# Optimization experiments

Measured on AMD Instinct MI355X. Metric: run time of the kernel, lower is better.

The kernel has to match this reference:

```python
import jax, jax.numpy as jnp
import numpy as np

B, S, H, NH = 4, 1024, 2048, 32
HD = H // NH
EPS = 1e-5

def layer_norm(x, w, b):
    mu = jnp.mean(x, axis=-1, keepdims=True)
    var = jnp.mean(jnp.square(x - mu), axis=-1, keepdims=True)
    return (x - mu) * jax.lax.rsqrt(var + EPS) * w + b

def setup_inputs() -> dict:
    key = jax.random.key(0)
    ks = jax.random.split(key, 8)
    s = 0.02
    inp = {
        'hidden_states': jax.random.normal(ks[0], (B, S, H), jnp.float32),
        'mask': jnp.tril(jnp.ones((S, S), jnp.float32))[None, None],  # causal 0/1
        'ln1_w': jnp.ones((H,), jnp.float32), 'ln1_b': jnp.zeros((H,), jnp.float32),
        'w_qkv': s * jax.random.normal(ks[1], (H, 3 * H), jnp.float32),
        'b_qkv': jnp.zeros((3 * H,), jnp.float32),
        'w_dense': s * jax.random.normal(ks[2], (H, H), jnp.float32),
        'b_dense': jnp.zeros((H,), jnp.float32),
        'ln3_w': jnp.ones((H,), jnp.float32), 'ln3_b': jnp.zeros((H,), jnp.float32),
        'ln2_w': jnp.ones((H,), jnp.float32), 'ln2_b': jnp.zeros((H,), jnp.float32),
        'w_h4h': s * jax.random.normal(ks[3], (H, 4 * H), jnp.float32),
        'b_h4h': jnp.zeros((4 * H,), jnp.float32),
        'w_4hh': s * jax.random.normal(ks[4], (4 * H, H), jnp.float32),
        'b_4hh': jnp.zeros((H,), jnp.float32),
        'ln4_w': jnp.ones((H,), jnp.float32), 'ln4_b': jnp.zeros((H,), jnp.float32),
    }
    return inp

def _layer(hidden_states, mask, ln1_w, ln1_b, w_qkv, b_qkv, w_dense, b_dense,
           ln3_w, ln3_b, ln2_w, ln2_b, w_h4h, b_h4h, w_4hh, b_4hh, ln4_w, ln4_b):
    # --- input LN ---
    x1 = layer_norm(hidden_states, ln1_w, ln1_b)
    # --- self attention ---
    qkv = x1 @ w_qkv + b_qkv                              # [B,S,3H]
    q, k, v = jnp.split(qkv, 3, axis=-1)
    def heads(t):  # [B,S,H] -> [B,NH,S,HD]
        return t.reshape(B, S, NH, HD).transpose(0, 2, 1, 3)
    q, k, v = heads(q), heads(k), heads(v)
    scores = jnp.einsum('bnqd,bnkd->bnqk', q / jnp.sqrt(jnp.float32(HD)), k)
    scores = scores * mask - 10000.0 * (1.0 - mask)
    probs = jax.nn.softmax(scores, axis=-1)
    ctx = jnp.einsum('bnqk,bnkd->bnqd', probs, v)
    ctx = ctx.transpose(0, 2, 1, 3).reshape(B, S, H)
    attn_out = ctx @ w_dense + b_dense
    # sandwich LN on attention output
    attn_out = layer_norm(attn_out, ln3_w, ln3_b)
    ln_input = hidden_states + attn_out
    # --- MLP ---
    x2 = layer_norm(ln_input, ln2_w, ln2_b)
    inter = jax.nn.gelu(x2 @ w_h4h + b_h4h, approximate=True)
    mlp_out = inter @ w_4hh + b_4hh
    mlp_out = layer_norm(mlp_out, ln4_w, ln4_b)
    return ln_input + mlp_out

def reference(hidden_states, mask, ln1_w, ln1_b, w_qkv, b_qkv, w_dense, b_dense,
              ln3_w, ln3_b, ln2_w, ln2_b, w_h4h, b_h4h, w_4hh, b_4hh, ln4_w, ln4_b):
    return _layer(hidden_states, mask, ln1_w, ln1_b, w_qkv, b_qkv, w_dense, b_dense,
                  ln3_w, ln3_b, ln2_w, ln2_b, w_h4h, b_h4h, w_4hh, b_4hh, ln4_w, ln4_b)
```

## Files before the change

### kernel.cpp

```cpp
#include <hip/hip_runtime.h>
#include <cstdint>
#include <cstddef>

typedef __bf16 bf16_t;
typedef __bf16 bf16x8 __attribute__((ext_vector_type(8)));
typedef float f32x4 __attribute__((ext_vector_type(4)));

#define BB 4
#define SS 1024
#define HH 2048
#define NHH 32
#define HDD 64
#define MTOK 4096

static constexpr size_t OFF_WQKV   = 0;
static constexpr size_t OFF_WDENSE = 25165824;
static constexpr size_t OFF_WH4H   = 33554432;
static constexpr size_t OFF_W4HH   = 67108864;
static constexpr size_t OFF_X1     = 100663296;
static constexpr size_t OFF_QKV    = 117440512;
static constexpr size_t OFF_ATTND2 = 150994944;
static constexpr size_t OFF_VT     = 167772160;
static constexpr size_t OFF_LNIN   = 184549376;
static constexpr size_t OFF_MLP    = 218103808;
static constexpr size_t OFF_MLP2   = 0;

__device__ __forceinline__ uint16_t f2bfu(float f) {
  union { float f; uint32_t u; } v; v.f = f;
  return (uint16_t)((v.u + 0x7FFFu + ((v.u >> 16) & 1u)) >> 16);
}
__device__ __forceinline__ bf16_t f2bf(float f) {
  union { uint16_t u; bf16_t b; } o; o.u = f2bfu(f);
  return o.b;
}

__device__ __forceinline__ void g2l16(const void* g, void* l) {
  __builtin_amdgcn_global_load_lds(
      (const __attribute__((address_space(1))) void*)g,
      (__attribute__((address_space(3))) void*)l, 16, 0, 0);
}

__global__ void convert_transpose_kernel(const float* __restrict__ W, bf16_t* __restrict__ WT,
                                         int K, int N) {
  __shared__ float t[32][33];
  const int n0 = blockIdx.x * 32;
  const int k0 = blockIdx.y * 32;
  const int tx = threadIdx.x, ty = threadIdx.y;
#pragma unroll
  for (int j = 0; j < 4; ++j)
    t[ty + j * 8][tx] = W[(size_t)(k0 + ty + j * 8) * N + n0 + tx];
  __syncthreads();
#pragma unroll
  for (int j = 0; j < 4; ++j)
    WT[(size_t)(n0 + ty + j * 8) * K + k0 + tx] = f2bf(t[tx][ty + j * 8]);
}

__global__ void transpose_v_kernel(const bf16_t* __restrict__ v, bf16_t* __restrict__ vT) {
  __shared__ bf16_t t[32][33];
  const int s0 = blockIdx.x * 32;
  const int d0 = blockIdx.y * 32;
  const size_t bh = blockIdx.z;
  const int tx = threadIdx.x, ty = threadIdx.y;
  const bf16_t* src = v + bh * (size_t)SS * HDD;
#pragma unroll
  for (int j = 0; j < 4; ++j)
    t[ty + j * 8][tx] = src[(size_t)(s0 + ty + j * 8) * HDD + d0 + tx];
  __syncthreads();
  bf16_t* dst = vT + bh * (size_t)HDD * SS;
#pragma unroll
  for (int j = 0; j < 4; ++j)
    dst[(size_t)(d0 + ty + j * 8) * SS + s0 + tx] = t[tx][ty + j * 8];
}

__device__ __forceinline__ void block_reduce2(float& s, float& ss) {
#pragma unroll
  for (int o = 32; o > 0; o >>= 1) {
    s += __shfl_down(s, o, 64);
    ss += __shfl_down(ss, o, 64);
  }
  __shared__ float red[8];
  const int wave = threadIdx.x >> 6;
  const int lane = threadIdx.x & 63;
  if (lane == 0) { red[wave] = s; red[4 + wave] = ss; }
  __syncthreads();
  s = red[0] + red[1] + red[2] + red[3];
  ss = red[4] + red[5] + red[6] + red[7];
  __syncthreads();
}

__device__ __forceinline__ void load8(const float* base, int tid, float* v) {
  float4 a = ((const float4*)base)[tid];
  float4 b = ((const float4*)base)[tid + 256];
  v[0] = a.x; v[1] = a.y; v[2] = a.z; v[3] = a.w;
  v[4] = b.x; v[5] = b.y; v[6] = b.z; v[7] = b.w;
}
__device__ __forceinline__ void store8f(float* base, int tid, const float* v) {
  ((float4*)base)[tid] = make_float4(v[0], v[1], v[2], v[3]);
  ((float4*)base)[tid + 256] = make_float4(v[4], v[5], v[6], v[7]);
}
__device__ __forceinline__ void store8bf(bf16_t* base, int tid, const float* v) {
  ushort4 o0 = {f2bfu(v[0]), f2bfu(v[1]), f2bfu(v[2]), f2bfu(v[3])};
  ushort4 o1 = {f2bfu(v[4]), f2bfu(v[5]), f2bfu(v[6]), f2bfu(v[7])};
  ((ushort4*)base)[tid] = o0;
  ((ushort4*)base)[tid + 256] = o1;
}
__device__ __forceinline__ void row_stats(const float* v, float& mean, float& inv) {
  float s = 0.f, ss = 0.f;
#pragma unroll
  for (int i = 0; i < 8; ++i) { s += v[i]; ss += v[i] * v[i]; }
  block_reduce2(s, ss);
  mean = s * (1.0f / 2048.0f);
  float var = ss * (1.0f / 2048.0f) - mean * mean;
  inv = rsqrtf(var + 1e-5f);
}

__global__ __launch_bounds__(256) void ln1_kernel(const float* __restrict__ x,
                                                  const float* __restrict__ w,
                                                  const float* __restrict__ b,
                                                  bf16_t* __restrict__ out) {
  const int row = blockIdx.x, tid = threadIdx.x;
  float v[8], wv[8], bv[8], o[8];
  load8(x + (size_t)row * HH, tid, v);
  float mean, inv;
  row_stats(v, mean, inv);
  load8(w, tid, wv);
  load8(b, tid, bv);
#pragma unroll
  for (int i = 0; i < 8; ++i) o[i] = (v[i] - mean) * inv * wv[i] + bv[i];
  store8bf(out + (size_t)row * HH, tid, o);
}

__global__ __launch_bounds__(256) void fuse_mid_kernel(
    const float* __restrict__ ad, const float* __restrict__ ad2,
    const float* __restrict__ hid,
    const float* __restrict__ w3, const float* __restrict__ b3,
    const float* __restrict__ w2, const float* __restrict__ b2,
    float* __restrict__ lnin, bf16_t* __restrict__ x2) {
  const int row = blockIdx.x, tid = threadIdx.x;
  float a[8], a2[8], h[8], wv[8], bv[8], l[8], o[8];
  load8(ad + (size_t)row * HH, tid, a);
  load8(ad2 + (size_t)row * HH, tid, a2);
#pragma unroll
  for (int i = 0; i < 8; ++i) a[i] += a2[i];
  float mean3, inv3;
  row_stats(a, mean3, inv3);
  load8(hid + (size_t)row * HH, tid, h);
  load8(w3, tid, wv);
  load8(b3, tid, bv);
#pragma unroll
  for (int i = 0; i < 8; ++i) l[i] = h[i] + (a[i] - mean3) * inv3 * wv[i] + bv[i];
  store8f(lnin + (size_t)row * HH, tid, l);
  float mean2, inv2;
  row_stats(l, mean2, inv2);
  load8(w2, tid, wv);
  load8(b2, tid, bv);
#pragma unroll
  for (int i = 0; i < 8; ++i) o[i] = (l[i] - mean2) * inv2 * wv[i] + bv[i];
  store8bf(x2 + (size_t)row * HH, tid, o);
}

__global__ __launch_bounds__(256) void fuse_out_kernel(
    const float* __restrict__ mlp, const float* __restrict__ mlp2,
    const float* __restrict__ lnin,
    const float* __restrict__ w4, const float* __restrict__ b4,
    float* __restrict__ out) {
  const int row = blockIdx.x, tid = threadIdx.x;
  float m[8], m2[8], l[8], wv[8], bv[8], o[8];
  load8(mlp + (size_t)row * HH, tid, m);
  load8(mlp2 + (size_t)row * HH, tid, m2);
#pragma unroll
  for (int i = 0; i < 8; ++i) m[i] += m2[i];
  float mean4, inv4;
  row_stats(m, mean4, inv4);
  load8(lnin + (size_t)row * HH, tid, l);
  load8(w4, tid, wv);
  load8(b4, tid, bv);
#pragma unroll
  for (int i = 0; i < 8; ++i) o[i] = l[i] + (m[i] - mean4) * inv4 * wv[i] + bv[i];
  store8f(out + (size_t)row * HH, tid, o);
}

#define MFMA16(a, b, cc) __builtin_amdgcn_mfma_f32_16x16x32_bf16(a, b, cc, 0, 0, 0)

#define STAGE(ISB, BUF, HALF, KT) do {                                              \
    const char* _s = ((ISB) ? bPan : aPan) + (size_t)((HALF) * 128) * ldb +         \
                     (size_t)(KT) * 128 + scb;                                      \
    char* _d = lds + ((ISB) ? 65536 : 0) + (BUF) * 32768 + (HALF) * 16384 +         \
               wave * 1024;                                                         \
    g2l16(_s + (size_t)srow * ldb, _d);                                             \
    g2l16(_s + (size_t)(srow + 64) * ldb, _d + 8192);                               \
  } while (0)

#define LDA(BUF, MQ)                                                                \
  _Pragma("unroll") for (int mf = 0; mf < 4; ++mf) {                                \
    const char* _p = aRd + (BUF) * 32768 + (MQ) * 8192 + mf * 2048;                 \
    aR[mf * 2]     = *(const bf16x8*)(_p + colK0);                                  \
    aR[mf * 2 + 1] = *(const bf16x8*)(_p + colK1);                                  \
  }

#define LDB(BR, BUF, NQ)                                                            \
  _Pragma("unroll") for (int nf = 0; nf < 2; ++nf) {                                \
    const char* _p = bRd + (BUF) * 32768 + (NQ) * 4096 + nf * 2048;                 \
    BR[nf * 2]     = *(const bf16x8*)(_p + colK0);                                  \
    BR[nf * 2 + 1] = *(const bf16x8*)(_p + colK1);                                  \
  }

#define MMA(MQ, NQ, BR)                                                             \
  _Pragma("unroll") for (int mf = 0; mf < 4; ++mf)                                  \
  _Pragma("unroll") for (int nf = 0; nf < 2; ++nf)                                  \
  _Pragma("unroll") for (int ks = 0; ks < 2; ++ks)                                  \
    acc[(MQ) * 4 + mf][(NQ) * 2 + nf] =                                             \
        MFMA16(aR[mf * 2 + ks], BR[nf * 2 + ks], acc[(MQ) * 4 + mf][(NQ) * 2 + nf]);

#define BARS()                                                                      \
  __builtin_amdgcn_sched_barrier(0);                                                \
  __builtin_amdgcn_s_barrier();                                                     \
  __builtin_amdgcn_s_setprio(1);

#define ENDP()                                                                      \
  __builtin_amdgcn_s_setprio(0);                                                    \
  __builtin_amdgcn_sched_barrier(0);                                                \
  __builtin_amdgcn_s_barrier();

template <int EPI, int SPLITK>
__global__ __launch_bounds__(512, 2) void gemm256(
    const bf16_t* __restrict__ A, const bf16_t* __restrict__ BT,
    const float* __restrict__ bias, void* __restrict__ out0, void* __restrict__ out1,
    const int M, const int N, const int Keff, const int ldK) {
  __shared__ alignas(16) char lds[131072];
  const int tid = threadIdx.x;
  const int wave = tid >> 6, lane = tid & 63;
  const int wm = wave >> 2, wn = wave & 3;
  const int c = lane & 15, g = lane >> 4;

  const int nwg = gridDim.x;
  int bid = (blockIdx.x & 7) * (nwg >> 3) + (blockIdx.x >> 3);
  const int nm = M >> 8;
  int slice = 0;
  if (SPLITK == 2) {
    const int per = nm * (N >> 8);
    slice = bid >= per;
    bid -= slice * per;
  }
  const int mt = bid % nm, nt = bid / nm;

  const size_t ldb = (size_t)ldK * 2;
  const char* aPan = (const char*)A + (size_t)(mt * 256) * ldb + (size_t)(slice * Keff) * 2;
  const char* bPan = (const char*)BT + (size_t)(nt * 256) * ldb + (size_t)(slice * Keff) * 2;

  const int srow = tid >> 3;
  const int scb = ((tid & 7) << 4) ^ ((srow & 7) << 4);

  const int x4 = (c & 7) << 4;
  const int colK0 = (g * 16) ^ x4;
  const int colK1 = (64 + g * 16) ^ x4;
  const char* aRd = lds + wm * 16384 + c * 128;
  const char* bRd = lds + 65536 + (wn >> 1) * 16384 + ((wn & 1) * 64 + c) * 128;

  f32x4 acc[8][4] = {};
  bf16x8 aR[8], b0R[4], b1R[4];

  const int NITER = Keff >> 7;
  const int NT2 = NITER * 2;

  STAGE(1, 0, 0, 0); STAGE(1, 0, 1, 0); STAGE(0, 0, 0, 0); STAGE(0, 0, 1, 0);
  STAGE(1, 1, 0, 1); STAGE(1, 1, 1, 1);
  asm volatile("s_waitcnt vmcnt(4)" ::: "memory");
  __builtin_amdgcn_sched_barrier(0);
  __builtin_amdgcn_s_barrier();

  for (int it = 0; it < NITER; ++it) {
    const int ktb = 2 * it + 1;
    int kt2 = 2 * it + 2; if (kt2 >= NT2) kt2 = 0;
    int kt3 = 2 * it + 3; if (kt3 >= NT2) kt3 = 0;
    LDA(0, 0); LDB(b0R, 0, 0); STAGE(0, 1, 0, ktb);
    BARS(); MMA(0, 0, b0R); ENDP();
    LDB(b1R, 0, 1); STAGE(0, 1, 1, ktb);
    BARS(); MMA(0, 1, b1R); ENDP();
    LDA(0, 1); STAGE(1, 0, 0, kt2);
    BARS(); MMA(1, 1, b1R); ENDP();
    STAGE(1, 0, 1, kt2);
    asm volatile("s_waitcnt vmcnt(4)" ::: "memory");
    BARS(); MMA(1, 0, b0R); ENDP();
    LDA(1, 0); LDB(b0R, 1, 0); STAGE(0, 0, 0, kt2);
    BARS(); MMA(0, 0, b0R); ENDP();
    LDB(b1R, 1, 1); STAGE(0, 0, 1, kt2);
    BARS(); MMA(0, 1, b1R); ENDP();
    LDA(1, 1); STAGE(1, 1, 0, kt3);
    BARS(); MMA(1, 1, b1R); ENDP();
    STAGE(1, 1, 1, kt3);
    asm volatile("s_waitcnt vmcnt(4)" ::: "memory");
    BARS(); MMA(1, 0, b0R); ENDP();
  }

  const int rowb = mt * 256 + wm * 128 + g * 4;
  const int colb = nt * 256 + wn * 64 + c;
  if constexpr (EPI == 0) {
    float* o = (float*)(slice ? out1 : out0);
#pragma unroll
    for (int nf = 0; nf < 4; ++nf) {
      const int col = colb + nf * 16;
      const float bv = (slice == 0) ? bias[col] : 0.0f;
#pragma unroll
      for (int mf = 0; mf < 8; ++mf) {
        const int r = rowb + mf * 16;
#pragma unroll
        for (int e = 0; e < 4; ++e)
          o[(size_t)(r + e) * N + col] = acc[mf][nf][e] + bv;
      }
    }
  } else if constexpr (EPI == 1) {
    bf16_t* o = (bf16_t*)out0;
#pragma unroll
    for (int nf = 0; nf < 4; ++nf) {
      const int col = colb + nf * 16;
      const float bv = bias[col];
      const int which = col >> 11;
      const int hh = (col & 2047) >> 6;
      const int dd = col & 63;
#pragma unroll
      for (int mf = 0; mf < 8; ++mf) {
        const int r = rowb + mf * 16;
#pragma unroll
        for (int e = 0; e < 4; ++e) {
          const int rr2 = r + e;
          const int bb = rr2 >> 10;
          const int sq = rr2 & 1023;
          o[(size_t)which * 8388608 +
            ((((size_t)bb * NHH + hh) * SS + sq) * HDD + dd)] = f2bf(acc[mf][nf][e] + bv);
        }
      }
    }
  } else {
    bf16_t* o = (bf16_t*)out0;
#pragma unroll
    for (int nf = 0; nf < 4; ++nf) {
      const int col = colb + nf * 16;
      const float bv = bias[col];
#pragma unroll
      for (int mf = 0; mf < 8; ++mf) {
        const int r = rowb + mf * 16;
#pragma unroll
        for (int e = 0; e < 4; ++e) {
          float u = acc[mf][nf][e] + bv;
          float cc2 = 0.7978845608f * (u + 0.044715f * u * u * u);
          float ex = __expf(2.0f * cc2);
          float th = 1.0f - 2.0f / (ex + 1.0f);
          o[(size_t)(r + e) * N + col] = f2bf(0.5f * u * (1.0f + th));
        }
      }
    }
  }
}

__global__ __launch_bounds__(512) void attn_kernel(
    const bf16_t* __restrict__ q, const bf16_t* __restrict__ k,
    const bf16_t* __restrict__ vT, bf16_t* __restrict__ ctx) {
  __shared__ alignas(16) char Ksm[8192];
  __shared__ alignas(16) char Vsm[8192];
  __shared__ alignas(16) char Psm[16384];

  const int id = blockIdx.x;
  const int qt = 7 - (id >> 7);
  const int bh = id & 127;
  const int tid = threadIdx.x;
  const int wave = tid >> 6;
  const int lane = tid & 63;
  const int q0 = qt * 128;
  const int q0w = q0 + wave * 16;
  const int c = lane & 15;
  const int g = lane >> 4;

  const bf16_t* qb = q + ((size_t)bh * SS + q0w) * HDD;
  const bf16x8 qa0 = *(const bf16x8*)(qb + c * HDD + g * 8);
  const bf16x8 qa1 = *(const bf16x8*)(qb + c * HDD + 32 + g * 8);

  f32x4 o[4] = {};
  float mrow[4], lrow[4];
#pragma unroll
  for (int e = 0; e < 4; ++e) { mrow[e] = -1e30f; lrow[e] = 0.0f; }

  const int sr = tid >> 3;
  const int sgb = ((tid & 7) * 16) ^ ((sr & 7) << 4);
  const char* kgb = (const char*)(k + (size_t)bh * SS * HDD);
  const char* vgb = (const char*)(vT + (size_t)bh * HDD * SS);
  char* kdst = Ksm + wave * 1024;
  char* vdst = Vsm + wave * 1024;
  char* Pw = Psm + wave * 2048;

  const int ntiles = (q0 + 128) >> 6;

  for (int t = 0; t < ntiles; ++t) {
    const int kb = t * 64;
    g2l16(kgb + (size_t)(kb + sr) * 128 + sgb, kdst);
    g2l16(vgb + (size_t)sr * 2048 + (size_t)kb * 2 + sgb, vdst);
    __syncthreads();

    if (kb < q0w + 16) {
      f32x4 s[4] = {};
#pragma unroll
      for (int sub = 0; sub < 4; ++sub) {
        const int n = sub * 16 + c;
        const int x = (n & 7) << 4;
        bf16x8 kf0 = *(const bf16x8*)(Ksm + n * 128 + ((g * 16) ^ x));
        bf16x8 kf1 = *(const bf16x8*)(Ksm + n * 128 + ((64 + g * 16) ^ x));
        s[sub] = MFMA16(qa0, kf0, s[sub]);
        s[sub] = MFMA16(qa1, kf1, s[sub]);
      }
      const bool diag = (kb + 63 > q0w);
      float pv[4][4];
#pragma unroll
      for (int sub = 0; sub < 4; ++sub)
#pragma unroll
        for (int e = 0; e < 4; ++e) {
          float sv = s[sub][e] * 0.125f;
          if (diag && (kb + sub * 16 + c > q0w + g * 4 + e)) sv = -10000.0f;
          pv[sub][e] = sv;
        }
      float scale[4];
#pragma unroll
      for (int e = 0; e < 4; ++e) {
        float mx = fmaxf(fmaxf(pv[0][e], pv[1][e]), fmaxf(pv[2][e], pv[3][e]));
        mx = fmaxf(mx, __shfl_xor(mx, 1, 64));
        mx = fmaxf(mx, __shfl_xor(mx, 2, 64));
        mx = fmaxf(mx, __shfl_xor(mx, 4, 64));
        mx = fmaxf(mx, __shfl_xor(mx, 8, 64));
        const float mnew = fmaxf(mrow[e], mx);
        scale[e] = __expf(mrow[e] - mnew);
        mrow[e] = mnew;
      }
#pragma unroll
      for (int e = 0; e < 4; ++e) {
        const int row = g * 4 + e;
        const int xr = (row & 7) << 4;
        float sum = 0.0f;
#pragma unroll
        for (int sub = 0; sub < 4; ++sub) {
          float p = __expf(pv[sub][e] - mrow[e]);
          sum += p;
          const int cb = (sub * 16 + c) * 2;
          *(bf16_t*)(Pw + row * 128 + (cb ^ xr)) = f2bf(p);
        }
        sum += __shfl_xor(sum, 1, 64);
        sum += __shfl_xor(sum, 2, 64);
        sum += __shfl_xor(sum, 4, 64);
        sum += __shfl_xor(sum, 8, 64);
        lrow[e] = lrow[e] * scale[e] + sum;
      }
#pragma unroll
      for (int d = 0; d < 4; ++d)
#pragma unroll
        for (int e = 0; e < 4; ++e) o[d][e] *= scale[e];
      const int xa = (c & 7) << 4;
      bf16x8 pa0 = *(const bf16x8*)(Pw + c * 128 + ((g * 16) ^ xa));
      bf16x8 pa1 = *(const bf16x8*)(Pw + c * 128 + ((64 + g * 16) ^ xa));
#pragma unroll
      for (int d = 0; d < 4; ++d) {
        const int n = d * 16 + c;
        const int xv = (n & 7) << 4;
        bf16x8 vf0 = *(const bf16x8*)(Vsm + n * 128 + ((g * 16) ^ xv));
        bf16x8 vf1 = *(const bf16x8*)(Vsm + n * 128 + ((64 + g * 16) ^ xv));
        o[d] = MFMA16(pa0, vf0, o[d]);
        o[d] = MFMA16(pa1, vf1, o[d]);
      }
    }
    __syncthreads();
  }

  const int b = bh >> 5, h = bh & 31;
#pragma unroll
  for (int e = 0; e < 4; ++e) {
    const int qrow = q0w + g * 4 + e;
    const float inv = 1.0f / lrow[e];
#pragma unroll
    for (int d = 0; d < 4; ++d)
      ctx[((size_t)b * SS + qrow) * HH + h * 64 + d * 16 + c] = f2bf(o[d][e] * inv);
  }
}

extern "C" void kernel_launch(void* const* d_in, const int* in_sizes, int n_in,
                              void* d_out, int out_size, void* d_ws, size_t ws_size,
                              hipStream_t stream) {
  const float* hidden = (const float*)d_in[0];
  const float* ln1w = (const float*)d_in[2];
  const float* ln1b = (const float*)d_in[3];
  const float* wqkv = (const float*)d_in[4];
  const float* bqkv = (const float*)d_in[5];
  const float* wdense = (const float*)d_in[6];
  const float* bdense = (const float*)d_in[7];
  const float* ln3w = (const float*)d_in[8];
  const float* ln3b = (const float*)d_in[9];
  const float* ln2w = (const float*)d_in[10];
  const float* ln2b = (const float*)d_in[11];
  const float* wh4h = (const float*)d_in[12];
  const float* bh4h = (const float*)d_in[13];
  const float* w4hh = (const float*)d_in[14];
  const float* b4hh = (const float*)d_in[15];
  const float* ln4w = (const float*)d_in[16];
  const float* ln4b = (const float*)d_in[17];

  char* ws = (char*)d_ws;
  bf16_t* wqkvT = (bf16_t*)(ws + OFF_WQKV);
  bf16_t* wdenseT = (bf16_t*)(ws + OFF_WDENSE);
  bf16_t* wh4hT = (bf16_t*)(ws + OFF_WH4H);
  bf16_t* w4hhT = (bf16_t*)(ws + OFF_W4HH);
  bf16_t* x1 = (bf16_t*)(ws + OFF_X1);
  bf16_t* qkv = (bf16_t*)(ws + OFF_QKV);
  bf16_t* qp = qkv;
  bf16_t* kp = qkv + 8388608;
  bf16_t* vp = qkv + 2 * 8388608;
  bf16_t* vT = (bf16_t*)(ws + OFF_VT);
  bf16_t* ctx = (bf16_t*)(ws + OFF_X1);
  float* attnd = (float*)(ws + OFF_QKV);
  float* attnd2 = (float*)(ws + OFF_ATTND2);
  float* lnin = (float*)(ws + OFF_LNIN);
  bf16_t* x2 = (bf16_t*)(ws + OFF_X1);
  bf16_t* inter = (bf16_t*)(ws + OFF_QKV);
  float* mlp = (float*)(ws + OFF_MLP);
  float* mlp2 = (float*)(ws + OFF_MLP2);

  dim3 tb(32, 8);
  convert_transpose_kernel<<<dim3(6144 / 32, 2048 / 32), tb, 0, stream>>>(wqkv, wqkvT, 2048, 6144);
  convert_transpose_kernel<<<dim3(2048 / 32, 2048 / 32), tb, 0, stream>>>(wdense, wdenseT, 2048, 2048);
  convert_transpose_kernel<<<dim3(8192 / 32, 2048 / 32), tb, 0, stream>>>(wh4h, wh4hT, 2048, 8192);
  convert_transpose_kernel<<<dim3(2048 / 32, 8192 / 32), tb, 0, stream>>>(w4hh, w4hhT, 8192, 2048);

  ln1_kernel<<<MTOK, 256, 0, stream>>>(hidden, ln1w, ln1b, x1);

  gemm256<1, 1><<<dim3((6144 / 256) * (4096 / 256)), 512, 0, stream>>>(
      x1, wqkvT, bqkv, (void*)qp, nullptr, MTOK, 6144, 2048, 2048);

  transpose_v_kernel<<<dim3(SS / 32, HDD / 32, BB * NHH), tb, 0, stream>>>(vp, vT);

  attn_kernel<<<dim3(1024), 512, 0, stream>>>(qp, kp, vT, ctx);

  gemm256<0, 2><<<dim3((2048 / 256) * (4096 / 256) * 2), 512, 0, stream>>>(
      ctx, wdenseT, bdense, (void*)attnd, (void*)attnd2, MTOK, 2048, 1024, 2048);

  fuse_mid_kernel<<<MTOK, 256, 0, stream>>>(attnd, attnd2, hidden, ln3w, ln3b, ln2w, ln2b, lnin, x2);

  gemm256<2, 1><<<dim3((8192 / 256) * (4096 / 256)), 512, 0, stream>>>(
      x2, wh4hT, bh4h, (void*)inter, nullptr, MTOK, 8192, 2048, 2048);

  gemm256<0, 2><<<dim3((2048 / 256) * (4096 / 256) * 2), 512, 0, stream>>>(
      inter, w4hhT, b4hh, (void*)mlp, (void*)mlp2, MTOK, 2048, 4096, 8192);

  fuse_out_kernel<<<MTOK, 256, 0, stream>>>(mlp, mlp2, lnin, ln4w, ln4b, (float*)d_out);
}
```

Baseline: 639.8 us.

## Restructure GEMM LDS prefetch schedule to deeper full-tile lookahead

Reorders the global-to-LDS staging so that both A and B halves of a whole k-tile are prefetched one full tile ahead, with all eight stages issued in the prologue and a vmcnt(8) wait in place of vmcnt(4). The loads are grouped so they are issued in clusters after the phases that finish reading each buffer. The sched_barrier calls around the MFMA phases are removed, which gives the compiler more freedom to interleave instructions. The aim is to hide global memory latency better. The cost is more loads in flight and a higher risk of LDS hazards if the buffer reuse order is wrong.

```diff
diff --git a/kernel.cpp b/kernel.cpp
--- a/kernel.cpp
+++ b/kernel.cpp
@@ -212,15 +212,15 @@
     acc[(MQ) * 4 + mf][(NQ) * 2 + nf] =                                             \
         MFMA16(aR[mf * 2 + ks], BR[nf * 2 + ks], acc[(MQ) * 4 + mf][(NQ) * 2 + nf]);
 
-#define BARS()                                                                      \
-  __builtin_amdgcn_sched_barrier(0);                                                \
+#define PH()                                                                        \
   __builtin_amdgcn_s_barrier();                                                     \
-  __builtin_amdgcn_s_setprio(1);
-
-#define ENDP()                                                                      \
+  __builtin_amdgcn_s_setprio(1)
+
+#define PE()                                                                        \
   __builtin_amdgcn_s_setprio(0);                                                    \
-  __builtin_amdgcn_sched_barrier(0);                                                \
-  __builtin_amdgcn_s_barrier();
+  __builtin_amdgcn_s_barrier()
+
+#define VM8() asm volatile("s_waitcnt vmcnt(8)" ::: "memory")
 
 template <int EPI, int SPLITK>
 __global__ __launch_bounds__(512, 2) void gemm256(
@@ -263,34 +263,34 @@
   const int NITER = Keff >> 7;
   const int NT2 = NITER * 2;
 
-  STAGE(1, 0, 0, 0); STAGE(1, 0, 1, 0); STAGE(0, 0, 0, 0); STAGE(0, 0, 1, 0);
+  STAGE(0, 0, 0, 0); STAGE(0, 0, 1, 0);
+  STAGE(1, 0, 0, 0); STAGE(1, 0, 1, 0);
+  STAGE(0, 1, 0, 1); STAGE(0, 1, 1, 1);
   STAGE(1, 1, 0, 1); STAGE(1, 1, 1, 1);
-  asm volatile("s_waitcnt vmcnt(4)" ::: "memory");
-  __builtin_amdgcn_sched_barrier(0);
+  VM8();
   __builtin_amdgcn_s_barrier();
 
   for (int it = 0; it < NITER; ++it) {
-    const int ktb = 2 * it + 1;
-    int kt2 = 2 * it + 2; if (kt2 >= NT2) kt2 = 0;
-    int kt3 = 2 * it + 3; if (kt3 >= NT2) kt3 = 0;
-    LDA(0, 0); LDB(b0R, 0, 0); STAGE(0, 1, 0, ktb);
-    BARS(); MMA(0, 0, b0R); ENDP();
-    LDB(b1R, 0, 1); STAGE(0, 1, 1, ktb);
-    BARS(); MMA(0, 1, b1R); ENDP();
-    LDA(0, 1); STAGE(1, 0, 0, kt2);
-    BARS(); MMA(1, 1, b1R); ENDP();
-    STAGE(1, 0, 1, kt2);
-    asm volatile("s_waitcnt vmcnt(4)" ::: "memory");
-    BARS(); MMA(1, 0, b0R); ENDP();
-    LDA(1, 0); LDB(b0R, 1, 0); STAGE(0, 0, 0, kt2);
-    BARS(); MMA(0, 0, b0R); ENDP();
-    LDB(b1R, 1, 1); STAGE(0, 0, 1, kt2);
-    BARS(); MMA(0, 1, b1R); ENDP();
-    LDA(1, 1); STAGE(1, 1, 0, kt3);
-    BARS(); MMA(1, 1, b1R); ENDP();
-    STAGE(1, 1, 1, kt3);
-    asm volatile("s_waitcnt vmcnt(4)" ::: "memory");
-    BARS(); MMA(1, 0, b0R); ENDP();
+    int kt2 = 2 * it + 2; if (kt2 >= NT2) kt2 -= NT2;
+    int kt3 = 2 * it + 3; if (kt3 >= NT2) kt3 -= NT2;
+    LDA(0, 0); LDB(b0R, 0, 0);
+    PH(); MMA(0, 0, b0R); PE();
+    LDB(b1R, 0, 1);
+    PH(); MMA(0, 1, b1R); PE();
+    LDA(0, 1); STAGE(1, 0, 0, kt2); STAGE(1, 0, 1, kt2);
+    PH(); MMA(1, 1, b1R); PE();
+    STAGE(0, 0, 0, kt2); STAGE(0, 0, 1, kt2);
+    VM8();
+    PH(); MMA(1, 0, b0R); PE();
+    LDA(1, 0); LDB(b0R, 1, 0);
+    PH(); MMA(0, 0, b0R); PE();
+    LDB(b1R, 1, 1);
+    PH(); MMA(0, 1, b1R); PE();
+    LDA(1, 1); STAGE(1, 1, 0, kt3); STAGE(1, 1, 1, kt3);
+    PH(); MMA(1, 1, b1R); PE();
+    STAGE(0, 1, 0, kt3); STAGE(0, 1, 1, kt3);
+    VM8();
+    PH(); MMA(1, 0, b0R); PE();
   }
 
   const int rowb = mt * 256 + wm * 128 + g * 4;
```

Measured after the change: 663.1 us. 1.04x slower.
